# Optimization experiments

Measured on AMD Instinct MI355X. Metric: run time of the kernel, lower is better.

The kernel has to match this reference:

```python
import jax, jax.numpy as jnp
import numpy as np

B, S, H, N_NODE = 4096, 50, 128, 50000
STDV = 1.0 / np.sqrt(H)


def _uniform(key, shape):
    return jax.random.uniform(key, shape, jnp.float32, -STDV, STDV)


def setup_inputs() -> dict:
    key = jax.random.key(0)
    ks = jax.random.split(key, 14)
    inputs = jax.random.randint(ks[0], (B, S), 0, N_NODE)
    A = jax.random.uniform(ks[1], (B, S, 2 * S), jnp.float32)
    return {
        "inputs": inputs,
        "A": A,
        "emb": _uniform(ks[2], (N_NODE, H)),
        "W_in": _uniform(ks[3], (H, H)),
        "b_in": _uniform(ks[4], (H,)),
        "W_out": _uniform(ks[5], (H, H)),
        "b_out": _uniform(ks[6], (H,)),
        "w_ih": _uniform(ks[7], (3 * H, 2 * H)),
        "b_ih": _uniform(ks[8], (3 * H,)),
        "w_hh": _uniform(ks[9], (3 * H, H)),
        "b_hh": _uniform(ks[10], (3 * H,)),
        "b_iah": _uniform(ks[11], (H,)),
        "b_oah": _uniform(ks[12], (H,)),
    }


def reference(inputs, A, emb, W_in, b_in, W_out, b_out, w_ih, b_ih, w_hh, b_hh, b_iah, b_oah):
    hidden = emb[inputs]                      # [B,S,H]
    s = A.shape[1]
    A_in, A_out = A[:, :, :s], A[:, :, s:2 * s]
    # edge-wise linear projections then adjacency aggregation
    h_in = jnp.einsum('bsh,gh->bsg', hidden, W_in) + b_in
    h_out = jnp.einsum('bsh,gh->bsg', hidden, W_out) + b_out
    input_in = jnp.matmul(A_in, h_in) + b_iah    # [B,S,H]
    input_out = jnp.matmul(A_out, h_out) + b_oah # [B,S,H]
    inp = jnp.concatenate([input_in, input_out], axis=2)  # [B,S,2H]
    gi = jnp.einsum('bsi,gi->bsg', inp, w_ih) + b_ih       # [B,S,3H]
    gh = jnp.einsum('bsh,gh->bsg', hidden, w_hh) + b_hh    # [B,S,3H]
    i_r, i_i, i_n = jnp.split(gi, 3, axis=2)
    h_r, h_i, h_n = jnp.split(gh, 3, axis=2)
    resetgate = jax.nn.sigmoid(i_r + h_r)
    inputgate = jax.nn.sigmoid(i_i + h_i)
    newgate = jnp.tanh(i_n + resetgate * h_n)
    hy = newgate + inputgate * (hidden - newgate)
    return hy
```

## Files before the change

### kernel.cpp

```cpp
#include <hip/hip_runtime.h>
#include <stdint.h>

typedef unsigned short u16;
typedef unsigned int u32;
typedef unsigned long long u64;
typedef __attribute__((ext_vector_type(4))) float f32x4;
typedef __attribute__((ext_vector_type(8))) short s16x8;
typedef __attribute__((ext_vector_type(4))) u16 u16x4;
typedef __attribute__((ext_vector_type(2))) u32 u32x2;
typedef __attribute__((ext_vector_type(4))) u32 u32x4;

#define NS 50
#define NH 128

#define HT_OFF 0
#define M_OFF  16384
#define A2_OFF 41984
#define RS_OFF 47584
#define LDS_TOTAL 48096

__device__ __forceinline__ u16 f2bf(float f) {
  u32 u = __builtin_bit_cast(u32, f);
  u32 r = (u + 0x7FFFu + ((u >> 16) & 1u)) >> 16;
  return (u16)r;
}
__device__ __forceinline__ float bf2f(u16 u) {
  return __builtin_bit_cast(float, (u32)u << 16);
}
__device__ __forceinline__ float sigm(float x) { return 1.0f / (1.0f + __expf(-x)); }
__device__ __forceinline__ float tanh_(float x) { return 1.0f - 2.0f / (1.0f + __expf(2.0f * x)); }
__device__ __forceinline__ s16x8 pack8(f32x4 a, f32x4 b) {
  s16x8 r;
  r[0] = (short)f2bf(a[0]); r[1] = (short)f2bf(a[1]);
  r[2] = (short)f2bf(a[2]); r[3] = (short)f2bf(a[3]);
  r[4] = (short)f2bf(b[0]); r[5] = (short)f2bf(b[1]);
  r[6] = (short)f2bf(b[2]); r[7] = (short)f2bf(b[3]);
  return r;
}
__device__ __forceinline__ s16x8 afrag_tr2(const unsigned char* p) {
  u32x2 a, b;
  asm volatile(
      "ds_read_b64_tr_b16 %0, %2\n\t"
      "ds_read_b64_tr_b16 %1, %2 offset:128\n\t"
      "s_waitcnt lgkmcnt(0)"
      : "=&v"(a), "=&v"(b)
      : "v"((const __attribute__((address_space(3))) unsigned char*)p)
      : "memory");
  __builtin_amdgcn_sched_barrier(0);
  u32x4 t; t[0] = a[0]; t[1] = a[1]; t[2] = b[0]; t[3] = b[1];
  return __builtin_bit_cast(s16x8, t);
}

__global__ __launch_bounds__(256) void k1_prep(
    const float* __restrict__ W_in, const float* __restrict__ b_in,
    const float* __restrict__ W_out, const float* __restrict__ b_out,
    const float* __restrict__ w_ih, const float* __restrict__ b_ih,
    const float* __restrict__ w_hh,
    const float* __restrict__ b_iah, const float* __restrict__ b_oah,
    u16* __restrict__ UcatT, float* __restrict__ cvec)
{
  int e = blockIdx.x * 256 + threadIdx.x;
  if (e < 147456) {
    int j = e >> 7, k = e & 127;
    float s = 0.f;
    if (j < 768) {
      const float* wr = w_ih + (size_t)(j < 384 ? j : j - 384) * 256 + (j < 384 ? 0 : 128);
      const float* Wc = (j < 384 ? W_in : W_out) + k;
      #pragma unroll 8
      for (int h = 0; h < 128; ++h) s += wr[h] * Wc[h * 128];
    } else {
      s = w_hh[(size_t)(j - 768) * 128 + k];
    }
    UcatT[e] = f2bf(s);
  } else if (e < 147456 + 1152) {
    int e2 = e - 147456;
    int which = e2 / 384, g = e2 - which * 384;
    const float* wr = w_ih + (size_t)g * 256;
    float s = 0.f;
    if (which == 0) { for (int h = 0; h < 128; ++h) s += wr[h] * b_in[h]; }
    else if (which == 1) { for (int h = 0; h < 128; ++h) s += wr[128 + h] * b_out[h]; }
    else {
      for (int h = 0; h < 128; ++h) s += wr[h] * b_iah[h] + wr[128 + h] * b_oah[h];
      s += b_ih[g];
    }
    cvec[which * 384 + g] = s;
  }
}

__global__ __launch_bounds__(256, 2) void k3_main(
    const int* __restrict__ inputs, const float* __restrict__ A,
    const u16* __restrict__ UcatT, const float* __restrict__ cvec,
    const float* __restrict__ emb, const float* __restrict__ b_hh,
    float* __restrict__ out)
{
  __shared__ __align__(128) unsigned char Sb[LDS_TOTAL];

  const int tid = threadIdx.x;
  const int b = blockIdx.x;
  const int w = tid >> 6, l = tid & 63;
  const int l16 = l & 15, g4 = l >> 4;

  const float* Ab = A + (size_t)b * (NS * 2 * NS);
  const int* inp = inputs + b * NS;
  float* outB = out + (size_t)b * NS * NH;
  float* rs = (float*)(Sb + RS_OFF);

  if (tid < 100) {
    int s = tid < 50 ? tid : tid - 50;
    const float* ap = Ab + s * 100;
    float sum;
    if (tid < 50) {
      f32x4 a4 = *(const f32x4*)ap;
      #pragma unroll
      for (int q = 1; q < 12; ++q) a4 += *(const f32x4*)(ap + q * 4);
      f32x4 vt = *(const f32x4*)(ap + 48);
      sum = (a4[0] + a4[1]) + (a4[2] + a4[3]) + vt[0] + vt[1];
    } else {
      f32x4 vt = *(const f32x4*)(ap + 48);
      f32x4 a4 = *(const f32x4*)(ap + 52);
      #pragma unroll
      for (int q = 1; q < 12; ++q) a4 += *(const f32x4*)(ap + 52 + q * 4);
      sum = (a4[0] + a4[1]) + (a4[2] + a4[3]) + vt[2] + vt[3];
    }
    rs[(tid < 50 ? 0 : 64) + s] = sum;
  }

  if (tid < 224) {
    int hc = tid / 28, q = tid - hc * 28;
    u32x4 z = {0, 0, 0, 0};
    *(u32x4*)(Sb + HT_OFF + hc * 2048 + 1600 + q * 16) = z;
  }
  if (tid < 150) {
    int row = tid / 3, d = tid - row * 3;
    *(u32*)(Sb + A2_OFF + row * 112 + 100 + d * 4) = 0u;
  }

  #pragma unroll
  for (int i = 0; i < 7; ++i) {
    int slot = i * 256 + tid;
    if (slot < 1600) {
      int t = slot >> 5, hch = slot & 31;
      int node = inp[t];
      f32x4 v = *(const f32x4*)(emb + (size_t)node * NH + hch * 4);
      u32 lo = (u32)f2bf(v[0]) | ((u32)f2bf(v[1]) << 16);
      u32 hi = (u32)f2bf(v[2]) | ((u32)f2bf(v[3]) << 16);
      u32x2 pv = {lo, hi};
      *(u32x2*)(Sb + HT_OFF + (hch >> 2) * 2048 + (t >> 2) * 128 + (t & 3) * 32 + (hch & 3) * 8) = pv;
    }
  }

  #pragma unroll
  for (int i = 0; i < 3; ++i) {
    int slot = i * 256 + tid;
    if (slot < 650) {
      int row = slot / 13, q = slot - row * 13;
      f32x4 v = *(const f32x4*)(Ab + row * 100 + 48 + q * 4);
      u32 lo = (u32)f2bf(v[0]) | ((u32)f2bf(v[1]) << 16);
      u32 hi = (u32)f2bf(v[2]) | ((u32)f2bf(v[3]) << 16);
      unsigned char* rp = Sb + A2_OFF + row * 112;
      if (q == 0) {
        *(u32*)(rp) = hi;
      } else {
        *(u32*)(rp + (q * 8 - 4)) = lo;
        *(u32*)(rp + (q * 8)) = hi;
      }
    }
  }

  s16x8 BfIn[4][2];
  #pragma unroll
  for (int nt = 0; nt < 4; ++nt) {
    int s = nt * 16 + l16; if (s > NS - 1) s = NS - 1;
    const float* ap = Ab + s * 100;
    {
      f32x4 x = *(const f32x4*)(ap + g4 * 8);
      f32x4 y = *(const f32x4*)(ap + g4 * 8 + 4);
      BfIn[nt][0] = pack8(x, y);
    }
    {
      f32x4 x = *(const f32x4*)(ap + 32 + g4 * 8);
      f32x4 y = *(const f32x4*)(ap + 32 + g4 * 8 + 4);
      int tb = 32 + g4 * 8;
      #pragma unroll
      for (int j = 0; j < 4; ++j) {
        if (tb + j >= NS) x[j] = 0.f;
        if (tb + 4 + j >= NS) y[j] = 0.f;
      }
      BfIn[nt][1] = pack8(x, y);
    }
  }
  __syncthreads();

  const s16x8 zero8 = {0, 0, 0, 0, 0, 0, 0, 0};

  #pragma unroll
  for (int ht2 = 0; ht2 < 2; ++ht2) {
    const int htile = w * 2 + ht2;
    f32x4 accM[2][4] = {};
    #pragma unroll
    for (int kt = 0; kt < 2; ++kt) {
      s16x8 Af = afrag_tr2(Sb + HT_OFF + htile * 2048 + (kt * 8 + 2 * g4) * 128 + l16 * 8);
      #pragma unroll
      for (int nt = 0; nt < 4; ++nt)
        accM[0][nt] = __builtin_amdgcn_mfma_f32_16x16x32_bf16(Af, BfIn[nt][kt], accM[0][nt], 0, 0, 0);
      #pragma unroll
      for (int nt = 0; nt < 4; ++nt) {
        int s = nt * 16 + l16; if (s > NS - 1) s = NS - 1;
        int off = kt * 64 + g4 * 16;
        s16x8 Bo = zero8;
        if (off < 112) Bo = *(const s16x8*)(Sb + A2_OFF + s * 112 + off);
        accM[1][nt] = __builtin_amdgcn_mfma_f32_16x16x32_bf16(Af, Bo, accM[1][nt], 0, 0, 0);
      }
    }
    #pragma unroll
    for (int mo = 0; mo < 2; ++mo)
      #pragma unroll
      for (int nt = 0; nt < 4; ++nt) {
        int s = nt * 16 + l16;
        if (s < NS) {
          u32 colb = (u32)((mo * 128 + htile * 16 + g4 * 4) * 2);
          u32 swz = (u32)((s & 7) << 4);
          u32 lo = (u32)f2bf(accM[mo][nt][0]) | ((u32)f2bf(accM[mo][nt][1]) << 16);
          u32 hi = (u32)f2bf(accM[mo][nt][2]) | ((u32)f2bf(accM[mo][nt][3]) << 16);
          u32x2 pv = {lo, hi};
          *(u32x2*)(Sb + M_OFF + s * 512 + (colb ^ swz)) = pv;
        }
      }
  }
  __syncthreads();

  #pragma unroll
  for (int ht = 0; ht < 2; ++ht) {
    const int hb = w * 32 + ht * 16;
    f32x4 acc2[3][4] = {};
    f32x4 acc3[3][4] = {};
    __builtin_amdgcn_s_setprio(1);
    #pragma unroll
    for (int kt = 0; kt < 8; ++kt) {
      s16x8 Bm[4];
      #pragma unroll
      for (int nt = 0; nt < 4; ++nt) {
        int s = nt * 16 + l16; if (s > NS - 1) s = NS - 1;
        Bm[nt] = *(const s16x8*)(Sb + M_OFF + s * 512 +
                                 ((u32)(kt * 64 + g4 * 16) ^ (u32)((s & 7) << 4)));
      }
      #pragma unroll
      for (int gate = 0; gate < 3; ++gate) {
        int j = (kt < 4 ? 0 : 384) + gate * 128 + hb + l16;
        s16x8 Au = *(const s16x8*)(UcatT + (size_t)j * 128 + (kt & 3) * 32 + g4 * 8);
        #pragma unroll
        for (int nt = 0; nt < 4; ++nt)
          acc2[gate][nt] = __builtin_amdgcn_mfma_f32_16x16x32_bf16(Au, Bm[nt], acc2[gate][nt], 0, 0, 0);
      }
    }
    #pragma unroll
    for (int kt = 0; kt < 4; ++kt) {
      s16x8 Bh[4];
      #pragma unroll
      for (int nt = 0; nt < 4; ++nt) {
        int s = nt * 16 + l16; if (s > NS - 1) s = NS - 1;
        int h = kt * 32 + g4 * 8;
        Bh[nt] = *(const s16x8*)(Sb + HT_OFF + (h >> 4) * 2048 + (s >> 2) * 128 +
                                 (s & 3) * 32 + (h & 15) * 2);
      }
      #pragma unroll
      for (int gate = 0; gate < 3; ++gate) {
        int j = 768 + gate * 128 + hb + l16;
        s16x8 Au = *(const s16x8*)(UcatT + (size_t)j * 128 + kt * 32 + g4 * 8);
        #pragma unroll
        for (int nt = 0; nt < 4; ++nt)
          acc3[gate][nt] = __builtin_amdgcn_mfma_f32_16x16x32_bf16(Au, Bh[nt], acc3[gate][nt], 0, 0, 0);
      }
    }
    __builtin_amdgcn_s_setprio(0);

    const int h0 = hb + g4 * 4;
    f32x4 cin[3], cou[3], cz[3], bh[3];
    #pragma unroll
    for (int gate = 0; gate < 3; ++gate) {
      int g = gate * 128 + h0;
      cin[gate] = *(const f32x4*)(cvec + g);
      cou[gate] = *(const f32x4*)(cvec + 384 + g);
      cz[gate]  = *(const f32x4*)(cvec + 768 + g);
      bh[gate]  = *(const f32x4*)(b_hh + g);
    }
    #pragma unroll
    for (int nt = 0; nt < 4; ++nt) {
      int s = nt * 16 + l16;
      int sc = s > NS - 1 ? NS - 1 : s;
      u16x4 hid4 = *(const u16x4*)(Sb + HT_OFF + (h0 >> 4) * 2048 + (sc >> 2) * 128 +
                                   (sc & 3) * 32 + (h0 & 15) * 2);
      float rin = rs[sc], rou = rs[64 + sc];
      f32x4 res;
      #pragma unroll
      for (int r = 0; r < 4; ++r) {
        float gr_ = acc3[0][nt][r] + bh[0][r];
        float gi_ = acc3[1][nt][r] + bh[1][r];
        float gn_ = acc3[2][nt][r] + bh[2][r];
        float vr = acc2[0][nt][r] + rin * cin[0][r] + rou * cou[0][r] + cz[0][r] + gr_;
        float vi = acc2[1][nt][r] + rin * cin[1][r] + rou * cou[1][r] + cz[1][r] + gi_;
        float vn = acc2[2][nt][r] + rin * cin[2][r] + rou * cou[2][r] + cz[2][r];
        float rr = sigm(vr);
        float ii = sigm(vi);
        float nn = tanh_(vn + rr * gn_);
        res[r] = nn + ii * (bf2f(hid4[r]) - nn);
      }
      if (s < NS)
        *(f32x4*)(outB + (size_t)s * NH + h0) = res;
    }
  }
}

extern "C" void kernel_launch(void* const* d_in, const int* in_sizes, int n_in,
                              void* d_out, int out_size, void* d_ws, size_t ws_size,
                              hipStream_t stream) {
  const int*   inputs = (const int*)  d_in[0];
  const float* A      = (const float*)d_in[1];
  const float* emb    = (const float*)d_in[2];
  const float* W_in   = (const float*)d_in[3];
  const float* b_in   = (const float*)d_in[4];
  const float* W_out  = (const float*)d_in[5];
  const float* b_out  = (const float*)d_in[6];
  const float* w_ih   = (const float*)d_in[7];
  const float* b_ih   = (const float*)d_in[8];
  const float* w_hh   = (const float*)d_in[9];
  const float* b_hh   = (const float*)d_in[10];
  const float* b_iah  = (const float*)d_in[11];
  const float* b_oah  = (const float*)d_in[12];

  u16*   UcatT = (u16*)d_ws;
  float* cvec  = (float*)((char*)d_ws + 294912);

  k1_prep<<<dim3(581), dim3(256), 0, stream>>>(W_in, b_in, W_out, b_out, w_ih, b_ih,
                                               w_hh, b_iah, b_oah, UcatT, cvec);
  k3_main<<<dim3(4096), dim3(256), 0, stream>>>(inputs, A, UcatT, cvec, emb, b_hh,
                                                (float*)d_out);
}
```

Measured before the change: 243.9 us.

## Pre-pack weights in MFMA fragment order and read A_out fragments directly

The prep kernel now writes the fused weight matrix in a layout where each 16x32 MFMA A-fragment is a contiguous 1 KB chunk indexed by lane, so the main kernel's global weight loads become fully coalesced 16-byte-per-lane reads. The A_out staging through LDS (bf16 conversion, padding, and extra LDS region) is removed. B fragments for the out-adjacency MFMA are now built directly from global memory with 8-byte loads and bounds masking. This lowers LDS use and removes a staging pass, at the cost of more scattered, less aligned global loads of A inside the MFMA loop.

```diff
diff --git a/kernel.cpp b/kernel.cpp
--- a/kernel.cpp
+++ b/kernel.cpp
@@ -4,6 +4,7 @@
 typedef unsigned short u16;
 typedef unsigned int u32;
 typedef unsigned long long u64;
+typedef __attribute__((ext_vector_type(2))) float f32x2;
 typedef __attribute__((ext_vector_type(4))) float f32x4;
 typedef __attribute__((ext_vector_type(8))) short s16x8;
 typedef __attribute__((ext_vector_type(4))) u16 u16x4;
@@ -15,9 +16,8 @@
 
 #define HT_OFF 0
 #define M_OFF  16384
-#define A2_OFF 41984
-#define RS_OFF 47584
-#define LDS_TOTAL 48096
+#define RS_OFF 41984
+#define LDS_TOTAL 42496
 
 __device__ __forceinline__ u16 f2bf(float f) {
   u32 u = __builtin_bit_cast(u32, f);
@@ -50,6 +50,39 @@
   u32x4 t; t[0] = a[0]; t[1] = a[1]; t[2] = b[0]; t[3] = b[1];
   return __builtin_bit_cast(s16x8, t);
 }
+__device__ __forceinline__ s16x8 load_outfrag(const float* ap, int kbase) {
+  f32x4 x = {0.f, 0.f, 0.f, 0.f}, y = {0.f, 0.f, 0.f, 0.f};
+  const float* p = ap + 50 + kbase;
+  if (kbase <= 40) {
+    f32x2 a0 = *(const f32x2*)(p);
+    f32x2 a1 = *(const f32x2*)(p + 2);
+    f32x2 a2 = *(const f32x2*)(p + 4);
+    f32x2 a3 = *(const f32x2*)(p + 6);
+    x[0] = a0[0]; x[1] = a0[1]; x[2] = a1[0]; x[3] = a1[1];
+    y[0] = a2[0]; y[1] = a2[1]; y[2] = a3[0]; y[3] = a3[1];
+  } else if (kbase == 48) {
+    f32x2 a0 = *(const f32x2*)(p);
+    x[0] = a0[0]; x[1] = a0[1];
+  }
+  return pack8(x, y);
+}
+
+__device__ __forceinline__ int upack_pos(int j, int k) {
+  int kt4 = k >> 5, g4 = (k >> 3) & 3, e2 = k & 7;
+  int chunk;
+  if (j < 768) {
+    int big = j >= 384;
+    int jj = j - big * 384;
+    int gate = jj >> 7, jr = jj & 127;
+    chunk = ((big * 3 + gate) * 8 + (jr >> 4)) * 4 + kt4;
+    return chunk * 512 + ((g4 * 16 + (jr & 15)) * 8 + e2);
+  } else {
+    int jj = j - 768;
+    int gate = jj >> 7, jr = jj & 127;
+    chunk = 192 + (gate * 8 + (jr >> 4)) * 4 + kt4;
+    return chunk * 512 + ((g4 * 16 + (jr & 15)) * 8 + e2);
+  }
+}
 
 __global__ __launch_bounds__(256) void k1_prep(
     const float* __restrict__ W_in, const float* __restrict__ b_in,
@@ -57,7 +90,7 @@
     const float* __restrict__ w_ih, const float* __restrict__ b_ih,
     const float* __restrict__ w_hh,
     const float* __restrict__ b_iah, const float* __restrict__ b_oah,
-    u16* __restrict__ UcatT, float* __restrict__ cvec)
+    u16* __restrict__ Upk, float* __restrict__ cvec)
 {
   int e = blockIdx.x * 256 + threadIdx.x;
   if (e < 147456) {
@@ -71,7 +104,7 @@
     } else {
       s = w_hh[(size_t)(j - 768) * 128 + k];
     }
-    UcatT[e] = f2bf(s);
+    Upk[upack_pos(j, k)] = f2bf(s);
   } else if (e < 147456 + 1152) {
     int e2 = e - 147456;
     int which = e2 / 384, g = e2 - which * 384;
@@ -89,7 +122,7 @@
 
 __global__ __launch_bounds__(256, 2) void k3_main(
     const int* __restrict__ inputs, const float* __restrict__ A,
-    const u16* __restrict__ UcatT, const float* __restrict__ cvec,
+    const u16* __restrict__ Upk, const float* __restrict__ cvec,
     const float* __restrict__ emb, const float* __restrict__ b_hh,
     float* __restrict__ out)
 {
@@ -129,10 +162,6 @@
     int hc = tid / 28, q = tid - hc * 28;
     u32x4 z = {0, 0, 0, 0};
     *(u32x4*)(Sb + HT_OFF + hc * 2048 + 1600 + q * 16) = z;
-  }
-  if (tid < 150) {
-    int row = tid / 3, d = tid - row * 3;
-    *(u32*)(Sb + A2_OFF + row * 112 + 100 + d * 4) = 0u;
   }
 
   #pragma unroll
@@ -149,24 +178,6 @@
     }
   }
 
-  #pragma unroll
-  for (int i = 0; i < 3; ++i) {
-    int slot = i * 256 + tid;
-    if (slot < 650) {
-      int row = slot / 13, q = slot - row * 13;
-      f32x4 v = *(const f32x4*)(Ab + row * 100 + 48 + q * 4);
-      u32 lo = (u32)f2bf(v[0]) | ((u32)f2bf(v[1]) << 16);
-      u32 hi = (u32)f2bf(v[2]) | ((u32)f2bf(v[3]) << 16);
-      unsigned char* rp = Sb + A2_OFF + row * 112;
-      if (q == 0) {
-        *(u32*)(rp) = hi;
-      } else {
-        *(u32*)(rp + (q * 8 - 4)) = lo;
-        *(u32*)(rp + (q * 8)) = hi;
-      }
-    }
-  }
-
   s16x8 BfIn[4][2];
   #pragma unroll
   for (int nt = 0; nt < 4; ++nt) {
@@ -191,8 +202,6 @@
   }
   __syncthreads();
 
-  const s16x8 zero8 = {0, 0, 0, 0, 0, 0, 0, 0};
-
   #pragma unroll
   for (int ht2 = 0; ht2 < 2; ++ht2) {
     const int htile = w * 2 + ht2;
@@ -206,9 +215,7 @@
       #pragma unroll
       for (int nt = 0; nt < 4; ++nt) {
         int s = nt * 16 + l16; if (s > NS - 1) s = NS - 1;
-        int off = kt * 64 + g4 * 16;
-        s16x8 Bo = zero8;
-        if (off < 112) Bo = *(const s16x8*)(Sb + A2_OFF + s * 112 + off);
+        s16x8 Bo = load_outfrag(Ab + s * 100, kt * 32 + g4 * 8);
         accM[1][nt] = __builtin_amdgcn_mfma_f32_16x16x32_bf16(Af, Bo, accM[1][nt], 0, 0, 0);
       }
     }
@@ -229,9 +236,11 @@
   }
   __syncthreads();
 
+  const u16* upLane = Upk + (size_t)l * 8;
   #pragma unroll
   for (int ht = 0; ht < 2; ++ht) {
     const int hb = w * 32 + ht * 16;
+    const int js = w * 2 + ht;
     f32x4 acc2[3][4] = {};
     f32x4 acc3[3][4] = {};
     __builtin_amdgcn_s_setprio(1);
@@ -244,10 +253,11 @@
         Bm[nt] = *(const s16x8*)(Sb + M_OFF + s * 512 +
                                  ((u32)(kt * 64 + g4 * 16) ^ (u32)((s & 7) << 4)));
       }
+      const int big = kt >> 2, kt4 = kt & 3;
       #pragma unroll
       for (int gate = 0; gate < 3; ++gate) {
-        int j = (kt < 4 ? 0 : 384) + gate * 128 + hb + l16;
-        s16x8 Au = *(const s16x8*)(UcatT + (size_t)j * 128 + (kt & 3) * 32 + g4 * 8);
+        int chunk = ((big * 3 + gate) * 8 + js) * 4 + kt4;
+        s16x8 Au = *(const s16x8*)(upLane + chunk * 512);
         #pragma unroll
         for (int nt = 0; nt < 4; ++nt)
           acc2[gate][nt] = __builtin_amdgcn_mfma_f32_16x16x32_bf16(Au, Bm[nt], acc2[gate][nt], 0, 0, 0);
@@ -265,8 +275,8 @@
       }
       #pragma unroll
       for (int gate = 0; gate < 3; ++gate) {
-        int j = 768 + gate * 128 + hb + l16;
-        s16x8 Au = *(const s16x8*)(UcatT + (size_t)j * 128 + kt * 32 + g4 * 8);
+        int chunk = 192 + (gate * 8 + js) * 4 + kt;
+        s16x8 Au = *(const s16x8*)(upLane + chunk * 512);
         #pragma unroll
         for (int nt = 0; nt < 4; ++nt)
           acc3[gate][nt] = __builtin_amdgcn_mfma_f32_16x16x32_bf16(Au, Bh[nt], acc3[gate][nt], 0, 0, 0);
@@ -328,11 +338,11 @@
   const float* b_iah  = (const float*)d_in[11];
   const float* b_oah  = (const float*)d_in[12];
 
-  u16*   UcatT = (u16*)d_ws;
-  float* cvec  = (float*)((char*)d_ws + 294912);
+  u16*   Upk  = (u16*)d_ws;
+  float* cvec = (float*)((char*)d_ws + 294912);
 
   k1_prep<<<dim3(581), dim3(256), 0, stream>>>(W_in, b_in, W_out, b_out, w_ih, b_ih,
-                                               w_hh, b_iah, b_oah, UcatT, cvec);
-  k3_main<<<dim3(4096), dim3(256), 0, stream>>>(inputs, A, UcatT, cvec, emb, b_hh,
+                                               w_hh, b_iah, b_oah, Upk, cvec);
+  k3_main<<<dim3(4096), dim3(256), 0, stream>>>(inputs, A, Upk, cvec, emb, b_hh,
                                                 (float*)d_out);
 }
```

After: 223.9 us. -8.2%, faster.
